# Performance work log

Measured on AMD Instinct MI355X. Metric: run time of the kernel, lower is better.

Reference implementation:

```python
import jax, jax.numpy as jnp
import numpy as np

EMBED = 1024
HEADS = 16
HEAD_DIM = EMBED // HEADS


def setup_inputs() -> dict:
    key = jax.random.key(0)
    ks = jax.random.split(key, 7)
    B, Sd, Se = 4, 2048, 2048
    dec = jax.random.normal(ks[0], (B, Sd, EMBED), dtype=jnp.float32)
    enc = jax.random.normal(ks[1], (B, Se, EMBED), dtype=jnp.float32)
    scale = 1.0 / np.sqrt(EMBED)
    W_q = jax.random.normal(ks[2], (EMBED, EMBED), dtype=jnp.float32) * scale
    W_k = jax.random.normal(ks[3], (EMBED, EMBED), dtype=jnp.float32) * scale
    W_v = jax.random.normal(ks[4], (EMBED, EMBED), dtype=jnp.float32) * scale
    W_o = jax.random.normal(ks[5], (EMBED, EMBED), dtype=jnp.float32) * scale
    b_o = jax.random.normal(ks[6], (EMBED,), dtype=jnp.float32) * 0.01
    return {"decoder_input": dec, "encoder_output": enc,
            "W_q": W_q, "W_k": W_k, "W_v": W_v, "W_o": W_o, "b_o": b_o}


def reference(decoder_input, encoder_output, W_q, W_k, W_v, W_o, b_o):
    B, Sd, E = decoder_input.shape
    Se = encoder_output.shape[1]
    # projections (nn.Linear applies x @ W.T; here W is stored as [in, out])
    Q = (decoder_input @ W_q).reshape(B, Sd, HEADS, HEAD_DIM)
    K = (encoder_output @ W_k).reshape(B, Se, HEADS, HEAD_DIM)
    V = (encoder_output @ W_v).reshape(B, Se, HEADS, HEAD_DIM)
    # scores: [B, H, Sd, Se]
    scores = jnp.einsum('bqhd,bkhd->bhqk', Q, K) / jnp.sqrt(jnp.float32(HEAD_DIM))
    attn = jax.nn.softmax(scores, axis=-1)
    out = jnp.einsum('bhqk,bkhd->bqhd', attn, V).reshape(B, Sd, E)
    return out @ W_o + b_o
```

## Files before the change

kernel.cpp:

```cpp
#include <hip/hip_runtime.h>
#include <hip/hip_bf16.h>

namespace {

typedef __attribute__((ext_vector_type(8))) short bf16x8;
typedef __attribute__((ext_vector_type(4))) float f32x4;

constexpr int BATCH = 4;
constexpr int SEQ   = 2048;
constexpr int EMB   = 1024;
constexpr int NH    = 16;
constexpr int HD    = 64;
constexpr int MTOT  = BATCH * SEQ;
constexpr int KVW   = 2 * EMB;
constexpr float LOG2E = 1.44269504088896f;
constexpr float SOFTMAX_C = 16.0f;

__device__ __forceinline__ unsigned short f2bf(float x) {
    unsigned int u = __float_as_uint(x);
    u += 0x7fffu + ((u >> 16) & 1u);
    return (unsigned short)(u >> 16);
}

__device__ __forceinline__ unsigned pack_bf16(float lo, float hi) {
    unsigned ul = __float_as_uint(lo) + 0x8000u;
    unsigned uh = __float_as_uint(hi) + 0x8000u;
    return __builtin_amdgcn_perm(uh, ul, 0x07060302u);
}

__device__ __forceinline__ void gl_lds16(const void* g, void* l) {
    __builtin_amdgcn_global_load_lds(
        (const __attribute__((address_space(1))) unsigned int*)g,
        (__attribute__((address_space(3))) unsigned int*)l, 16, 0, 0);
}

__global__ __launch_bounds__(256)
void conv_bf16(const float* __restrict__ dec, const float* __restrict__ enc,
               unsigned short* __restrict__ decb, unsigned short* __restrict__ encb,
               int n4)
{
    int i = blockIdx.x * 256 + threadIdx.x;
    if (i >= n4) return;
    const float* src = blockIdx.y ? enc : dec;
    unsigned short* dst = blockIdx.y ? encb : decb;
    float4 v = ((const float4*)src)[i];
    ushort4 o;
    o.x = f2bf(v.x); o.y = f2bf(v.y); o.z = f2bf(v.z); o.w = f2bf(v.w);
    ((ushort4*)dst)[i] = o;
}

__global__ __launch_bounds__(256)
void wtrans(const float* __restrict__ W0, const float* __restrict__ W1,
            const float* __restrict__ W2, const float* __restrict__ W3,
            unsigned short* __restrict__ WtBase, float qscale)
{
    __shared__ __align__(16) unsigned short Ts[64][65];
    const int tid = threadIdx.x;
    const int z = blockIdx.z;
    const float* W = (z == 0) ? W0 : (z == 1) ? W1 : (z == 2) ? W2 : W3;
    unsigned short* Wt = WtBase + (size_t)z * EMB * EMB;
    const float scale = (z == 0) ? qscale : 1.0f;
    const int n0 = blockIdx.x * 64, k0 = blockIdx.y * 64;
    #pragma unroll
    for (int i = 0; i < 4; ++i) {
        int id = tid + i * 256;
        int r = id >> 4, q = id & 15;
        float4 v = *(const float4*)&W[(size_t)(k0 + r) * EMB + n0 + q * 4];
        Ts[q * 4 + 0][r] = f2bf(v.x * scale);
        Ts[q * 4 + 1][r] = f2bf(v.y * scale);
        Ts[q * 4 + 2][r] = f2bf(v.z * scale);
        Ts[q * 4 + 3][r] = f2bf(v.w * scale);
    }
    __syncthreads();
    #pragma unroll
    for (int i = 0; i < 4; ++i) {
        int id = tid + i * 256;
        int rn = id >> 4, q = id & 15;
        ushort4 o;
        o.x = Ts[rn][q * 4 + 0]; o.y = Ts[rn][q * 4 + 1];
        o.z = Ts[rn][q * 4 + 2]; o.w = Ts[rn][q * 4 + 3];
        *(ushort4*)&Wt[(size_t)(n0 + rn) * EMB + k0 + q * 4] = o;
    }
}

__global__ __launch_bounds__(256)
void vtrans(const unsigned short* __restrict__ V, unsigned short* __restrict__ Vt)
{
    __shared__ __align__(16) unsigned short Ts[64][72];
    const int tid = threadIdx.x;
    const int s0 = blockIdx.x * 64;
    const int bh = blockIdx.y, b = bh >> 4, h = bh & 15;
    #pragma unroll
    for (int it = 0; it < 2; ++it) {
        int id = tid + it * 256;
        int r = id >> 3, seg = id & 7;
        uint4 v = *(const uint4*)&V[(size_t)(b * SEQ + s0 + r) * KVW + h * HD + seg * 8];
        const unsigned short* pv = (const unsigned short*)&v;
        #pragma unroll
        for (int j = 0; j < 8; ++j) Ts[seg * 8 + j][r] = pv[j];
    }
    __syncthreads();
    #pragma unroll
    for (int it = 0; it < 2; ++it) {
        int id = tid + it * 256;
        int d = id >> 3, sg = id & 7;
        uint4 w = *(const uint4*)&Ts[d][sg * 8];
        *(uint4*)&Vt[((size_t)bh * HD + d) * SEQ + s0 + sg * 8] = w;
    }
}

template<bool OUT_BF16, bool BIAS>
__device__ __forceinline__
void gemm_body(const unsigned short* __restrict__ A, const unsigned short* __restrict__ Bt,
               const float* __restrict__ bias, void* __restrict__ Cout,
               int m0, int n0, int N, int Kd)
{
    __shared__ __align__(16) unsigned short As[2][128 * 32];
    __shared__ __align__(16) unsigned short Bs[2][128 * 32];
    const int tid  = threadIdx.x;
    const int lane = tid & 63, wave = tid >> 6;
    const int g = lane >> 4, c = lane & 15;
    const int wm = (wave & 1) * 64, wn = (wave >> 1) * 64;

    const int r0 = tid >> 2, s = tid & 3;
    const int sg = s ^ ((r0 + (r0 >> 2)) & 3);
    const unsigned short* ga0 = A  + (size_t)(m0 + r0)      * Kd + sg * 8;
    const unsigned short* ga1 = A  + (size_t)(m0 + r0 + 64) * Kd + sg * 8;
    const unsigned short* gb0 = Bt + (size_t)(n0 + r0)      * Kd + sg * 8;
    const unsigned short* gb1 = Bt + (size_t)(n0 + r0 + 64) * Kd + sg * 8;
    const int lo0 = tid * 8, lo1 = (256 + tid) * 8;

    const int cs = (c + (c >> 2)) & 3;

    f32x4 acc[4][4];
    #pragma unroll
    for (int i = 0; i < 4; ++i)
        #pragma unroll
        for (int j = 0; j < 4; ++j) acc[i][j] = (f32x4)0.0f;

    gl_lds16(ga0, &As[0][lo0]); gl_lds16(ga1, &As[0][lo1]);
    gl_lds16(gb0, &Bs[0][lo0]); gl_lds16(gb1, &Bs[0][lo1]);
    ga0 += 32; ga1 += 32; gb0 += 32; gb1 += 32;
    __syncthreads();

    const int KT = Kd / 32;
    for (int kt = 0; kt < KT; kt += 2) {
        #pragma unroll
        for (int h2 = 0; h2 < 2; ++h2) {
            const int k = kt + h2;
            if (k + 1 < KT) {
                gl_lds16(ga0, &As[h2 ^ 1][lo0]); gl_lds16(ga1, &As[h2 ^ 1][lo1]);
                gl_lds16(gb0, &Bs[h2 ^ 1][lo0]); gl_lds16(gb1, &Bs[h2 ^ 1][lo1]);
                ga0 += 32; ga1 += 32; gb0 += 32; gb1 += 32;
            }
            bf16x8 af[4], bfr[4];
            #pragma unroll
            for (int mt = 0; mt < 4; ++mt)
                af[mt]  = *(const bf16x8*)&As[h2][(wm + mt * 16 + c) * 32 + (g ^ cs) * 8];
            #pragma unroll
            for (int nt = 0; nt < 4; ++nt)
                bfr[nt] = *(const bf16x8*)&Bs[h2][(wn + nt * 16 + c) * 32 + (g ^ cs) * 8];
            #pragma unroll
            for (int mt = 0; mt < 4; ++mt)
                #pragma unroll
                for (int nt = 0; nt < 4; ++nt)
                    acc[mt][nt] = __builtin_amdgcn_mfma_f32_16x16x32_bf16(af[mt], bfr[nt], acc[mt][nt], 0, 0, 0);
            __syncthreads();
        }
    }

    #pragma unroll
    for (int mt = 0; mt < 4; ++mt) {
        #pragma unroll
        for (int nt = 0; nt < 4; ++nt) {
            int n = n0 + wn + nt * 16 + c;
            float bv = BIAS ? bias[n] : 0.0f;
            #pragma unroll
            for (int r = 0; r < 4; ++r) {
                int m = m0 + wm + mt * 16 + 4 * g + r;
                float v = acc[mt][nt][r] + bv;
                if (OUT_BF16) ((unsigned short*)Cout)[(size_t)m * N + n] = f2bf(v);
                else          ((float*)Cout)[(size_t)m * N + n] = v;
            }
        }
    }
}

__global__ __launch_bounds__(256)
void proj_fused(const unsigned short* __restrict__ decb, const unsigned short* __restrict__ encb,
                const unsigned short* __restrict__ WtBase,
                unsigned short* __restrict__ Qb, unsigned short* __restrict__ KVb)
{
    const int nt = blockIdx.x;
    const int m0 = blockIdx.y * 128;
    if (nt < 8) {
        gemm_body<true, false>(decb, WtBase, nullptr, Qb, m0, nt * 128, EMB, EMB);
    } else {
        gemm_body<true, false>(encb, WtBase + (size_t)EMB * EMB, nullptr, KVb,
                               m0, (nt - 8) * 128, KVW, EMB);
    }
}

__global__ __launch_bounds__(256)
void proj_out(const unsigned short* __restrict__ Ob, const unsigned short* __restrict__ WoT,
              const float* __restrict__ bo, float* __restrict__ out)
{
    gemm_body<false, true>(Ob, WoT, bo, out, blockIdx.y * 128, blockIdx.x * 128, EMB, EMB);
}

__global__ __launch_bounds__(256)
void attn(const unsigned short* __restrict__ Q, const unsigned short* __restrict__ KV,
          const unsigned short* __restrict__ Vt, unsigned short* __restrict__ O)
{
    __shared__ __align__(16) unsigned short Ks[2][64 * 64];
    __shared__ __align__(16) unsigned short Vs[2][64 * 64];
    __shared__ __align__(16) unsigned short Ps[4][32][72];

    const int tid  = threadIdx.x;
    const int lane = tid & 63, wave = tid >> 6;
    const int g = lane >> 4, c = lane & 15, c7 = c & 7;
    const int bh = blockIdx.y, b = bh >> 4, h = bh & 15;
    const int qw = blockIdx.x * 128 + wave * 32;

    const unsigned short* Qp0 = Q + (size_t)(b * SEQ + qw + c) * EMB + h * HD;
    const unsigned short* Qp1 = Qp0 + (size_t)16 * EMB;
    bf16x8 qb[2][2];
    qb[0][0] = *(const bf16x8*)(Qp0 + g * 8);
    qb[0][1] = *(const bf16x8*)(Qp0 + 32 + g * 8);
    qb[1][0] = *(const bf16x8*)(Qp1 + g * 8);
    qb[1][1] = *(const bf16x8*)(Qp1 + 32 + g * 8);

    const int r0 = tid >> 3, s8 = tid & 7;
    const int sg = s8 ^ (r0 & 7);
    const unsigned short* gK0 = KV + ((size_t)b * SEQ + r0) * KVW + h * HD + sg * 8;
    const unsigned short* gK1 = gK0 + (size_t)32 * KVW;
    const unsigned short* gV0 = Vt + (size_t)bh * HD * SEQ + (size_t)r0 * SEQ + sg * 8;
    const unsigned short* gV1 = gV0 + (size_t)32 * SEQ;
    const int lo0 = tid * 8, lo1 = (256 + tid) * 8;

    f32x4 oac[2][4];
    #pragma unroll
    for (int bd = 0; bd < 2; ++bd)
        #pragma unroll
        for (int dt = 0; dt < 4; ++dt) oac[bd][dt] = (f32x4)0.0f;
    float lrun[2] = {0.0f, 0.0f};
    const f32x4 minit = {-SOFTMAX_C, -SOFTMAX_C, -SOFTMAX_C, -SOFTMAX_C};

    gl_lds16(gK0, &Ks[0][lo0]); gl_lds16(gK1, &Ks[0][lo1]);
    gl_lds16(gV0, &Vs[0][lo0]); gl_lds16(gV1, &Vs[0][lo1]);
    gK0 += (size_t)64 * KVW; gK1 += (size_t)64 * KVW; gV0 += 64; gV1 += 64;
    __syncthreads();

    constexpr int T = SEQ / 64;
    for (int t = 0; t < T; t += 2) {
        #pragma unroll
        for (int h2 = 0; h2 < 2; ++h2) {
            const int tt = t + h2;
            if (tt + 1 < T) {
                gl_lds16(gK0, &Ks[h2 ^ 1][lo0]); gl_lds16(gK1, &Ks[h2 ^ 1][lo1]);
                gl_lds16(gV0, &Vs[h2 ^ 1][lo0]); gl_lds16(gV1, &Vs[h2 ^ 1][lo1]);
                gK0 += (size_t)64 * KVW; gK1 += (size_t)64 * KVW;
                gV0 += 64;               gV1 += 64;
            }

            f32x4 st[2][4];
            #pragma unroll
            for (int kt = 0; kt < 4; ++kt) {
                bf16x8 ka0 = *(const bf16x8*)&Ks[h2][(kt * 16 + c) * 64 + (g ^ c7) * 8];
                bf16x8 ka1 = *(const bf16x8*)&Ks[h2][(kt * 16 + c) * 64 + ((4 + g) ^ c7) * 8];
                #pragma unroll
                for (int bd = 0; bd < 2; ++bd) {
                    st[bd][kt] = __builtin_amdgcn_mfma_f32_16x16x32_bf16(ka0, qb[bd][0], minit, 0, 0, 0);
                    st[bd][kt] = __builtin_amdgcn_mfma_f32_16x16x32_bf16(ka1, qb[bd][1], st[bd][kt], 0, 0, 0);
                }
            }

            #pragma unroll
            for (int bd = 0; bd < 2; ++bd) {
                float ls = lrun[bd];
                #pragma unroll
                for (int kt = 0; kt < 4; ++kt) {
                    float p0 = __builtin_amdgcn_exp2f(st[bd][kt][0]);
                    float p1 = __builtin_amdgcn_exp2f(st[bd][kt][1]);
                    float p2 = __builtin_amdgcn_exp2f(st[bd][kt][2]);
                    float p3 = __builtin_amdgcn_exp2f(st[bd][kt][3]);
                    ls += (p0 + p1) + (p2 + p3);
                    uint2 u;
                    u.x = pack_bf16(p0, p1);
                    u.y = pack_bf16(p2, p3);
                    *(uint2*)&Ps[wave][bd * 16 + c][kt * 16 + 4 * g] = u;
                }
                lrun[bd] = ls;
            }

            bf16x8 pa[2][2];
            pa[0][0] = *(const bf16x8*)&Ps[wave][c][g * 8];
            pa[0][1] = *(const bf16x8*)&Ps[wave][c][32 + g * 8];
            pa[1][0] = *(const bf16x8*)&Ps[wave][16 + c][g * 8];
            pa[1][1] = *(const bf16x8*)&Ps[wave][16 + c][32 + g * 8];
            #pragma unroll
            for (int dt = 0; dt < 4; ++dt) {
                bf16x8 vb0 = *(const bf16x8*)&Vs[h2][(dt * 16 + c) * 64 + (g ^ c7) * 8];
                bf16x8 vb1 = *(const bf16x8*)&Vs[h2][(dt * 16 + c) * 64 + ((4 + g) ^ c7) * 8];
                #pragma unroll
                for (int bd = 0; bd < 2; ++bd) {
                    oac[bd][dt] = __builtin_amdgcn_mfma_f32_16x16x32_bf16(pa[bd][0], vb0, oac[bd][dt], 0, 0, 0);
                    oac[bd][dt] = __builtin_amdgcn_mfma_f32_16x16x32_bf16(pa[bd][1], vb1, oac[bd][dt], 0, 0, 0);
                }
            }

            __syncthreads();
        }
    }

    #pragma unroll
    for (int bd = 0; bd < 2; ++bd) {
        float v = lrun[bd];
        v += __shfl_xor(v, 16);
        v += __shfl_xor(v, 32);
        lrun[bd] = v;
    }
    #pragma unroll
    for (int bd = 0; bd < 2; ++bd) {
        unsigned short* Op = O + (size_t)(b * SEQ + qw + bd * 16) * EMB + h * HD;
        #pragma unroll
        for (int r = 0; r < 4; ++r) {
            float linv = 1.0f / __shfl(lrun[bd], 4 * g + r);
            #pragma unroll
            for (int dt = 0; dt < 4; ++dt)
                Op[(size_t)(4 * g + r) * EMB + dt * 16 + c] = f2bf(oac[bd][dt][r] * linv);
        }
    }
}

}

extern "C" void kernel_launch(void* const* d_in, const int* in_sizes, int n_in,
                              void* d_out, int out_size, void* d_ws, size_t ws_size,
                              hipStream_t stream)
{
    const float* dec = (const float*)d_in[0];
    const float* enc = (const float*)d_in[1];
    const float* Wq  = (const float*)d_in[2];
    const float* Wk  = (const float*)d_in[3];
    const float* Wv  = (const float*)d_in[4];
    const float* Wo  = (const float*)d_in[5];
    const float* bo  = (const float*)d_in[6];
    float* out = (float*)d_out;

    const size_t BIG = (size_t)MTOT * EMB;
    const size_t SML = (size_t)EMB * EMB;
    unsigned short* decb = (unsigned short*)d_ws;
    unsigned short* encb = decb + BIG;
    unsigned short* WqT  = encb + BIG;
    unsigned short* WoT  = WqT + 3 * SML;
    unsigned short* Qb   = WqT + 4 * SML;
    unsigned short* KVb  = Qb + BIG;
    unsigned short* Vtg  = KVb + 2 * BIG;
    unsigned short* Ob   = Vtg + BIG;

    dim3 blk(256);

    conv_bf16<<<dim3((unsigned)(BIG / 4 / 256), 2), blk, 0, stream>>>(
        dec, enc, decb, encb, (int)(BIG / 4));

    wtrans<<<dim3(16, 16, 4), blk, 0, stream>>>(Wq, Wk, Wv, Wo, WqT, 0.125f * LOG2E);

    proj_fused<<<dim3(24, MTOT / 128), blk, 0, stream>>>(decb, encb, WqT, Qb, KVb);

    vtrans<<<dim3(SEQ / 64, BATCH * NH), blk, 0, stream>>>(KVb + EMB, Vtg);

    attn<<<dim3(SEQ / 128, BATCH * NH), blk, 0, stream>>>(Qb, KVb, Vtg, Ob);

    proj_out<<<dim3(EMB / 128, MTOT / 128), blk, 0, stream>>>(Ob, WoT, bo, out);
}
```

Before: 334.8 us.

## Compute V transposed directly in projection GEMM and restructure attention inner loop

The V projection is now computed as Wv^T times enc^T, so the fused projection kernel writes V already transposed ([E, B*S]). This removes the separate vtrans kernel and its extra read and write of V. The attention loop now loads all K and V fragments up front and handles one 16-row query block at a time, which halves the P staging buffer. Launch bounds occupancy hints are also added. Holding the hoisted K/V fragments raises register pressure, and the transposed-V GEMM writes with a long stride.

```diff
diff --git a/kernel.cpp b/kernel.cpp
--- a/kernel.cpp
+++ b/kernel.cpp
@@ -12,7 +12,6 @@
 constexpr int NH    = 16;
 constexpr int HD    = 64;
 constexpr int MTOT  = BATCH * SEQ;
-constexpr int KVW   = 2 * EMB;
 constexpr float LOG2E = 1.44269504088896f;
 constexpr float SOFTMAX_C = 16.0f;
 
@@ -83,32 +82,6 @@
     }
 }
 
-__global__ __launch_bounds__(256)
-void vtrans(const unsigned short* __restrict__ V, unsigned short* __restrict__ Vt)
-{
-    __shared__ __align__(16) unsigned short Ts[64][72];
-    const int tid = threadIdx.x;
-    const int s0 = blockIdx.x * 64;
-    const int bh = blockIdx.y, b = bh >> 4, h = bh & 15;
-    #pragma unroll
-    for (int it = 0; it < 2; ++it) {
-        int id = tid + it * 256;
-        int r = id >> 3, seg = id & 7;
-        uint4 v = *(const uint4*)&V[(size_t)(b * SEQ + s0 + r) * KVW + h * HD + seg * 8];
-        const unsigned short* pv = (const unsigned short*)&v;
-        #pragma unroll
-        for (int j = 0; j < 8; ++j) Ts[seg * 8 + j][r] = pv[j];
-    }
-    __syncthreads();
-    #pragma unroll
-    for (int it = 0; it < 2; ++it) {
-        int id = tid + it * 256;
-        int d = id >> 3, sg = id & 7;
-        uint4 w = *(const uint4*)&Ts[d][sg * 8];
-        *(uint4*)&Vt[((size_t)bh * HD + d) * SEQ + s0 + sg * 8] = w;
-    }
-}
-
 template<bool OUT_BF16, bool BIAS>
 __device__ __forceinline__
 void gemm_body(const unsigned short* __restrict__ A, const unsigned short* __restrict__ Bt,
@@ -186,35 +159,41 @@
     }
 }
 
-__global__ __launch_bounds__(256)
+__global__ __launch_bounds__(256, 4)
 void proj_fused(const unsigned short* __restrict__ decb, const unsigned short* __restrict__ encb,
                 const unsigned short* __restrict__ WtBase,
-                unsigned short* __restrict__ Qb, unsigned short* __restrict__ KVb)
-{
-    const int nt = blockIdx.x;
-    const int m0 = blockIdx.y * 128;
-    if (nt < 8) {
-        gemm_body<true, false>(decb, WtBase, nullptr, Qb, m0, nt * 128, EMB, EMB);
+                unsigned short* __restrict__ Qb, unsigned short* __restrict__ Kb,
+                unsigned short* __restrict__ Vt2)
+{
+    const int id = blockIdx.x;
+    if (id < 512) {
+        gemm_body<true, false>(decb, WtBase, nullptr, Qb,
+                               (id >> 3) * 128, (id & 7) * 128, EMB, EMB);
+    } else if (id < 1024) {
+        const int j = id - 512;
+        gemm_body<true, false>(encb, WtBase + (size_t)EMB * EMB, nullptr, Kb,
+                               (j >> 3) * 128, (j & 7) * 128, EMB, EMB);
     } else {
-        gemm_body<true, false>(encb, WtBase + (size_t)EMB * EMB, nullptr, KVb,
-                               m0, (nt - 8) * 128, KVW, EMB);
-    }
-}
-
-__global__ __launch_bounds__(256)
+        const int j = id - 1024;
+        gemm_body<true, false>(WtBase + (size_t)2 * EMB * EMB, encb, nullptr, Vt2,
+                               (j & 7) * 128, (j >> 3) * 128, MTOT, EMB);
+    }
+}
+
+__global__ __launch_bounds__(256, 4)
 void proj_out(const unsigned short* __restrict__ Ob, const unsigned short* __restrict__ WoT,
               const float* __restrict__ bo, float* __restrict__ out)
 {
     gemm_body<false, true>(Ob, WoT, bo, out, blockIdx.y * 128, blockIdx.x * 128, EMB, EMB);
 }
 
-__global__ __launch_bounds__(256)
-void attn(const unsigned short* __restrict__ Q, const unsigned short* __restrict__ KV,
+__global__ __launch_bounds__(256, 3)
+void attn(const unsigned short* __restrict__ Q, const unsigned short* __restrict__ K,
           const unsigned short* __restrict__ Vt, unsigned short* __restrict__ O)
 {
     __shared__ __align__(16) unsigned short Ks[2][64 * 64];
     __shared__ __align__(16) unsigned short Vs[2][64 * 64];
-    __shared__ __align__(16) unsigned short Ps[4][32][72];
+    __shared__ __align__(16) unsigned short Ps[4][16][72];
 
     const int tid  = threadIdx.x;
     const int lane = tid & 63, wave = tid >> 6;
@@ -232,10 +211,10 @@
 
     const int r0 = tid >> 3, s8 = tid & 7;
     const int sg = s8 ^ (r0 & 7);
-    const unsigned short* gK0 = KV + ((size_t)b * SEQ + r0) * KVW + h * HD + sg * 8;
-    const unsigned short* gK1 = gK0 + (size_t)32 * KVW;
-    const unsigned short* gV0 = Vt + (size_t)bh * HD * SEQ + (size_t)r0 * SEQ + sg * 8;
-    const unsigned short* gV1 = gV0 + (size_t)32 * SEQ;
+    const unsigned short* gK0 = K + ((size_t)b * SEQ + r0) * EMB + h * HD + sg * 8;
+    const unsigned short* gK1 = gK0 + (size_t)32 * EMB;
+    const unsigned short* gV0 = Vt + (size_t)(h * HD + r0) * MTOT + b * SEQ + sg * 8;
+    const unsigned short* gV1 = gV0 + (size_t)32 * MTOT;
     const int lo0 = tid * 8, lo1 = (256 + tid) * 8;
 
     f32x4 oac[2][4];
@@ -248,7 +227,7 @@
 
     gl_lds16(gK0, &Ks[0][lo0]); gl_lds16(gK1, &Ks[0][lo1]);
     gl_lds16(gV0, &Vs[0][lo0]); gl_lds16(gV1, &Vs[0][lo1]);
-    gK0 += (size_t)64 * KVW; gK1 += (size_t)64 * KVW; gV0 += 64; gV1 += 64;
+    gK0 += (size_t)64 * EMB; gK1 += (size_t)64 * EMB; gV0 += 64; gV1 += 64;
     __syncthreads();
 
     constexpr int T = SEQ / 64;
@@ -259,53 +238,47 @@
             if (tt + 1 < T) {
                 gl_lds16(gK0, &Ks[h2 ^ 1][lo0]); gl_lds16(gK1, &Ks[h2 ^ 1][lo1]);
                 gl_lds16(gV0, &Vs[h2 ^ 1][lo0]); gl_lds16(gV1, &Vs[h2 ^ 1][lo1]);
-                gK0 += (size_t)64 * KVW; gK1 += (size_t)64 * KVW;
+                gK0 += (size_t)64 * EMB; gK1 += (size_t)64 * EMB;
                 gV0 += 64;               gV1 += 64;
             }
 
-            f32x4 st[2][4];
+            bf16x8 ka[4][2], vb[4][2];
             #pragma unroll
             for (int kt = 0; kt < 4; ++kt) {
-                bf16x8 ka0 = *(const bf16x8*)&Ks[h2][(kt * 16 + c) * 64 + (g ^ c7) * 8];
-                bf16x8 ka1 = *(const bf16x8*)&Ks[h2][(kt * 16 + c) * 64 + ((4 + g) ^ c7) * 8];
+                ka[kt][0] = *(const bf16x8*)&Ks[h2][(kt * 16 + c) * 64 + (g ^ c7) * 8];
+                ka[kt][1] = *(const bf16x8*)&Ks[h2][(kt * 16 + c) * 64 + ((4 + g) ^ c7) * 8];
+                vb[kt][0] = *(const bf16x8*)&Vs[h2][(kt * 16 + c) * 64 + (g ^ c7) * 8];
+                vb[kt][1] = *(const bf16x8*)&Vs[h2][(kt * 16 + c) * 64 + ((4 + g) ^ c7) * 8];
+            }
+
+            #pragma unroll
+            for (int bd = 0; bd < 2; ++bd) {
+                f32x4 st[4];
                 #pragma unroll
-                for (int bd = 0; bd < 2; ++bd) {
-                    st[bd][kt] = __builtin_amdgcn_mfma_f32_16x16x32_bf16(ka0, qb[bd][0], minit, 0, 0, 0);
-                    st[bd][kt] = __builtin_amdgcn_mfma_f32_16x16x32_bf16(ka1, qb[bd][1], st[bd][kt], 0, 0, 0);
+                for (int kt = 0; kt < 4; ++kt) {
+                    st[kt] = __builtin_amdgcn_mfma_f32_16x16x32_bf16(ka[kt][0], qb[bd][0], minit, 0, 0, 0);
+                    st[kt] = __builtin_amdgcn_mfma_f32_16x16x32_bf16(ka[kt][1], qb[bd][1], st[kt], 0, 0, 0);
                 }
-            }
-
-            #pragma unroll
-            for (int bd = 0; bd < 2; ++bd) {
                 float ls = lrun[bd];
                 #pragma unroll
                 for (int kt = 0; kt < 4; ++kt) {
-                    float p0 = __builtin_amdgcn_exp2f(st[bd][kt][0]);
-                    float p1 = __builtin_amdgcn_exp2f(st[bd][kt][1]);
-                    float p2 = __builtin_amdgcn_exp2f(st[bd][kt][2]);
-                    float p3 = __builtin_amdgcn_exp2f(st[bd][kt][3]);
+                    float p0 = __builtin_amdgcn_exp2f(st[kt][0]);
+                    float p1 = __builtin_amdgcn_exp2f(st[kt][1]);
+                    float p2 = __builtin_amdgcn_exp2f(st[kt][2]);
+                    float p3 = __builtin_amdgcn_exp2f(st[kt][3]);
                     ls += (p0 + p1) + (p2 + p3);
                     uint2 u;
                     u.x = pack_bf16(p0, p1);
                     u.y = pack_bf16(p2, p3);
-                    *(uint2*)&Ps[wave][bd * 16 + c][kt * 16 + 4 * g] = u;
+                    *(uint2*)&Ps[wave][c][kt * 16 + 4 * g] = u;
                 }
                 lrun[bd] = ls;
-            }
-
-            bf16x8 pa[2][2];
-            pa[0][0] = *(const bf16x8*)&Ps[wave][c][g * 8];
-            pa[0][1] = *(const bf16x8*)&Ps[wave][c][32 + g * 8];
-            pa[1][0] = *(const bf16x8*)&Ps[wave][16 + c][g * 8];
-            pa[1][1] = *(const bf16x8*)&Ps[wave][16 + c][32 + g * 8];
-            #pragma unroll
-            for (int dt = 0; dt < 4; ++dt) {
-                bf16x8 vb0 = *(const bf16x8*)&Vs[h2][(dt * 16 + c) * 64 + (g ^ c7) * 8];
-                bf16x8 vb1 = *(const bf16x8*)&Vs[h2][(dt * 16 + c) * 64 + ((4 + g) ^ c7) * 8];
+                bf16x8 pa0 = *(const bf16x8*)&Ps[wave][c][g * 8];
+                bf16x8 pa1 = *(const bf16x8*)&Ps[wave][c][32 + g * 8];
                 #pragma unroll
-                for (int bd = 0; bd < 2; ++bd) {
-                    oac[bd][dt] = __builtin_amdgcn_mfma_f32_16x16x32_bf16(pa[bd][0], vb0, oac[bd][dt], 0, 0, 0);
-                    oac[bd][dt] = __builtin_amdgcn_mfma_f32_16x16x32_bf16(pa[bd][1], vb1, oac[bd][dt], 0, 0, 0);
+                for (int dt = 0; dt < 4; ++dt) {
+                    oac[bd][dt] = __builtin_amdgcn_mfma_f32_16x16x32_bf16(pa0, vb[dt][0], oac[bd][dt], 0, 0, 0);
+                    oac[bd][dt] = __builtin_amdgcn_mfma_f32_16x16x32_bf16(pa1, vb[dt][1], oac[bd][dt], 0, 0, 0);
                 }
             }
 
@@ -355,9 +328,9 @@
     unsigned short* WqT  = encb + BIG;
     unsigned short* WoT  = WqT + 3 * SML;
     unsigned short* Qb   = WqT + 4 * SML;
-    unsigned short* KVb  = Qb + BIG;
-    unsigned short* Vtg  = KVb + 2 * BIG;
-    unsigned short* Ob   = Vtg + BIG;
+    unsigned short* Kb   = Qb + BIG;
+    unsigned short* Vt2  = Kb + BIG;
+    unsigned short* Ob   = Vt2 + BIG;
 
     dim3 blk(256);
 
@@ -366,11 +339,9 @@
 
     wtrans<<<dim3(16, 16, 4), blk, 0, stream>>>(Wq, Wk, Wv, Wo, WqT, 0.125f * LOG2E);
 
-    proj_fused<<<dim3(24, MTOT / 128), blk, 0, stream>>>(decb, encb, WqT, Qb, KVb);
-
-    vtrans<<<dim3(SEQ / 64, BATCH * NH), blk, 0, stream>>>(KVb + EMB, Vtg);
-
-    attn<<<dim3(SEQ / 128, BATCH * NH), blk, 0, stream>>>(Qb, KVb, Vtg, Ob);
-
-    proj_out<<<dim3(EMB / 128, MTOT / 128), blk, 0, stream>>>(Ob, WoT, bo, out);
-}
+    proj_fused<<<dim3(1536), blk, 0, stream>>>(decb, encb, WqT, Qb, Kb, Vt2);
+
+    attn<<<dim3(SEQ / 128, BATCH * NH), blk, 0, stream>>>(Qb, Kb, Vt2, Ob);
+
+    proj_out<<<dim3(EMB / 128, MTOT / 128), blk, 0, stream>>>(Ob, WqT + 3 * SML, bo, out);
+}
```

Result: slower. 405.3 us (+21.1%).
